# Performance work log

Hardware: AMD Instinct MI355X
Metric: run time of the kernel (lower is better)

Reference implementation:

```python
import jax, jax.numpy as jnp
import numpy as np

NUM_HEADS = 8
N_CHUNKS = 4


def _chunk_bounds(n, chunks):
    # replicate torch.chunk: chunk size = ceil(n/chunks), last chunk smaller
    cs = -(-n // chunks)
    return [min(i * cs, n) for i in range(chunks + 1)]


def setup_inputs() -> dict:
    key = jax.random.key(0)
    ks = jax.random.split(key, 9)
    dim, N, B = 512, 289, 256
    C = dim // 2
    H, d = NUM_HEADS, C // NUM_HEADS
    return {
        "x1": jax.random.normal(ks[0], (B, N, dim), jnp.float32),
        "x2": jax.random.normal(ks[1], (B, N, dim), jnp.float32),
        "W_reduce": jax.random.normal(ks[2], (dim, C), jnp.float32) * 0.02,
        "W_qkv": jax.random.normal(ks[3], (C, 3 * C), jnp.float32) * 0.02,
        "W_proj": jax.random.normal(ks[4], (C, dim), jnp.float32) * 0.02,
        "b_proj": jnp.zeros((dim,), jnp.float32),
        "w_ds": 1.0 + 0.02 * jax.random.normal(ks[5], (H, d), jnp.float32),
        "w_uds": 1.0 + 0.02 * jax.random.normal(ks[6], (H, d), jnp.float32),
        "b_uds": jnp.zeros((H, d), jnp.float32),
    }


def _branch(x, W_reduce, W_qkv, W_proj, b_proj, w_ds, w_uds, b_uds, use_ds):
    xr = x @ W_reduce                       # [B, N, C]
    B, N, C = xr.shape
    H = NUM_HEADS
    d = C // H
    scale = d ** -0.5
    qkv = (xr @ W_qkv).reshape(B, N, 3, H, d).transpose(2, 0, 3, 1, 4)  # [3,B,H,N,d]
    q, k, v = qkv[0], qkv[1], qkv[2]
    bounds = _chunk_bounds(N, N_CHUNKS)
    outs = []
    for i in range(N_CHUNKS):               # fixed 4-way chunking, per original
        s, e = bounds[i], bounds[i + 1]
        qc, kc, vc = q[:, :, s:e], k[:, :, s:e], v[:, :, s:e]
        if use_ds:
            # Distributive: learned per-head diagonal metric on head_dim, scale folded in
            attn = jnp.einsum('bhnd,bhmd->bhnm', qc * w_ds[None, :, None, :], kc) * scale
        else:
            # UnDistributive: learned per-head affine on q and k, then scaled dot-product
            qc = qc * w_uds[None, :, None, :] + b_uds[None, :, None, :]
            kc = kc * w_uds[None, :, None, :] + b_uds[None, :, None, :]
            attn = jnp.einsum('bhnd,bhmd->bhnm', qc, kc) * scale
        attn = jax.nn.softmax(attn, axis=-1)
        outs.append(jnp.einsum('bhnm,bhmd->bnhd', attn, vc))  # (attn @ v).transpose(1,2)
    o = jnp.concatenate(outs, axis=1).reshape(B, N, C)
    return o @ W_proj + b_proj


def reference(x1, x2, W_reduce, W_qkv, W_proj, b_proj, w_ds, w_uds, b_uds):
    y1 = _branch(x1, W_reduce, W_qkv, W_proj, b_proj, w_ds, w_uds, b_uds, use_ds=True)
    y2 = _branch(x2, W_reduce, W_qkv, W_proj, b_proj, w_ds, w_uds, b_uds, use_ds=False)
    return (y1, y2)
```

## Files before the change

kernel.cpp:

```cpp
#include <hip/hip_runtime.h>

typedef __bf16 bf16;
typedef bf16 bf16x4 __attribute__((ext_vector_type(4)));
typedef bf16 bf16x8 __attribute__((ext_vector_type(8)));
typedef float f32x4 __attribute__((ext_vector_type(4)));

#define LOG2E 1.4426950408889634f

__device__ __forceinline__ f32x4 mfma16(bf16x8 a, bf16x8 b, f32x4 c) {
    return __builtin_amdgcn_mfma_f32_16x16x32_bf16(a, b, c, 0, 0, 0);
}

__device__ __forceinline__ void async16(const void* g, void* l) {
    __builtin_amdgcn_global_load_lds(
        (const __attribute__((address_space(1))) void*)g,
        (__attribute__((address_space(3))) void*)l, 16, 0, 0);
}

__global__ __launch_bounds__(256) void prep_w(
    const float* __restrict__ Wr, const float* __restrict__ Wq,
    const float* __restrict__ w_ds, const float* __restrict__ w_uds,
    const float* __restrict__ b_uds,
    bf16* __restrict__ W1t, bf16* __restrict__ W2t, float* __restrict__ bias) {
    __shared__ float wq[256][17];
    const int t = threadIdx.x;
    const int k0 = blockIdx.x * 64, n0 = blockIdx.y * 16, z = blockIdx.z;
#pragma unroll
    for (int i = 0; i < 16; i++) {
        int c = i * 16 + (t >> 4);
        wq[c][t & 15] = Wq[c * 768 + n0 + (t & 15)];
    }
    __syncthreads();
    const int j = t & 15, n = n0 + j;
    const float rs = 0.17677669529663687f;
    float scale, bv;
    if (z == 0) {
        scale = (n < 256) ? w_ds[n] * rs : 1.f; bv = 0.f;
    } else if (n < 256) {
        scale = w_uds[n] * rs; bv = b_uds[n] * rs;
    } else if (n < 512) {
        scale = w_uds[n - 256]; bv = b_uds[n - 256];
    } else {
        scale = 1.f; bv = 0.f;
    }
    bf16* Wt = z ? W2t : W1t;
#pragma unroll 1
    for (int i = 0; i < 4; i++) {
        int k = k0 + (t >> 4) * 4 + i;
        float acc = 0.f;
        for (int c = 0; c < 256; c++) acc = fmaf(Wr[k * 256 + c], wq[c][j], acc);
        Wt[n * 512 + k] = (bf16)(acc * scale);
    }
    if (blockIdx.x == 0 && (t >> 4) == 0) bias[z * 768 + n] = bv;
}

__global__ void prep_wp(const float* __restrict__ Wp, bf16* __restrict__ Wpt) {
    const int n = blockIdx.x, k = threadIdx.x;
    Wpt[n * 256 + k] = (bf16)Wp[k * 512 + n];
}

__global__ __launch_bounds__(256) void gemm_qkv(
    const float* __restrict__ X, const bf16* __restrict__ Wt,
    const float* __restrict__ biasp, bf16* __restrict__ Out) {
    __shared__ __attribute__((aligned(16))) bf16 As[128 * 48];
    __shared__ __attribute__((aligned(16))) bf16 Bs[128 * 32];
    const int tid = threadIdx.x;
    const int lane = tid & 63, wave = tid >> 6;
    const int ln = lane & 15, quad = lane >> 4;
    const int bn = blockIdx.x * 128, bm = blockIdx.y * 128;
    const int wm = (wave & 1) * 64, wn = (wave >> 1) * 64;
    f32x4 acc[4][4] = {};
    float bi[4];
#pragma unroll
    for (int nt = 0; nt < 4; nt++) bi[nt] = biasp[bn + wn + nt * 16 + ln];
    const int brow = bn + wave * 32 + (lane >> 2);
    const int bcol0 = (lane & 3) * 8;
    bf16* bs_base0 = &Bs[(wave * 32) * 32];
    bf16* bs_base1 = &Bs[(wave * 32 + 16) * 32];

    for (int kb = 0; kb < 512; kb += 32) {
#pragma unroll
        for (int i = 0; i < 4; i++) {
            int idx = tid + i * 256;
            int row = idx >> 3;
            int c4 = (idx & 7) * 4;
            float4 v = *(const float4*)&X[(bm + row) * 512 + kb + c4];
            bf16x4 w = {(bf16)v.x, (bf16)v.y, (bf16)v.z, (bf16)v.w};
            *(bf16x4*)&As[row * 48 + c4] = w;
        }
        async16(&Wt[brow * 512 + kb + bcol0], bs_base0);
        async16(&Wt[(brow + 16) * 512 + kb + bcol0], bs_base1);
        __syncthreads();
        bf16x8 a[4], b[4];
#pragma unroll
        for (int mt = 0; mt < 4; mt++)
            a[mt] = *(const bf16x8*)&As[(wm + mt * 16 + ln) * 48 + quad * 8];
#pragma unroll
        for (int nt = 0; nt < 4; nt++)
            b[nt] = *(const bf16x8*)&Bs[(wn + nt * 16 + ln) * 32 + quad * 8];
#pragma unroll
        for (int mt = 0; mt < 4; mt++)
#pragma unroll
            for (int nt = 0; nt < 4; nt++)
                acc[mt][nt] = mfma16(a[mt], b[nt], acc[mt][nt]);
        __syncthreads();
    }
#pragma unroll
    for (int mt = 0; mt < 4; mt++)
#pragma unroll
        for (int nt = 0; nt < 4; nt++) {
            int col = bn + wn + nt * 16 + ln;
#pragma unroll
            for (int r = 0; r < 4; r++) {
                int row = bm + wm + mt * 16 + quad * 4 + r;
                Out[row * 768 + col] = (bf16)(acc[mt][nt][r] + bi[nt]);
            }
        }
}

__global__ __launch_bounds__(256) void gemm_proj(
    const bf16* __restrict__ A, const bf16* __restrict__ Wt,
    const float* __restrict__ bp, float* __restrict__ Y) {
    __shared__ __attribute__((aligned(16))) bf16 As[128 * 32];
    __shared__ __attribute__((aligned(16))) bf16 Bs[128 * 32];
    const int tid = threadIdx.x;
    const int lane = tid & 63, wave = tid >> 6;
    const int ln = lane & 15, quad = lane >> 4;
    const int bn = blockIdx.x * 128, bm = blockIdx.y * 128;
    const int wm = (wave & 1) * 64, wn = (wave >> 1) * 64;
    f32x4 acc[4][4] = {};
    float bi[4];
#pragma unroll
    for (int nt = 0; nt < 4; nt++) bi[nt] = bp[bn + wn + nt * 16 + ln];
    const int arow = bm + wave * 32 + (lane >> 2);
    const int brow = bn + wave * 32 + (lane >> 2);
    const int c0 = (lane & 3) * 8;
    bf16* as0 = &As[(wave * 32) * 32];
    bf16* as1 = &As[(wave * 32 + 16) * 32];
    bf16* bs0 = &Bs[(wave * 32) * 32];
    bf16* bs1 = &Bs[(wave * 32 + 16) * 32];

    for (int kb = 0; kb < 256; kb += 32) {
        async16(&A[arow * 256 + kb + c0], as0);
        async16(&A[(arow + 16) * 256 + kb + c0], as1);
        async16(&Wt[brow * 256 + kb + c0], bs0);
        async16(&Wt[(brow + 16) * 256 + kb + c0], bs1);
        __syncthreads();
        bf16x8 a[4], b[4];
#pragma unroll
        for (int mt = 0; mt < 4; mt++)
            a[mt] = *(const bf16x8*)&As[(wm + mt * 16 + ln) * 32 + quad * 8];
#pragma unroll
        for (int nt = 0; nt < 4; nt++)
            b[nt] = *(const bf16x8*)&Bs[(wn + nt * 16 + ln) * 32 + quad * 8];
#pragma unroll
        for (int mt = 0; mt < 4; mt++)
#pragma unroll
            for (int nt = 0; nt < 4; nt++)
                acc[mt][nt] = mfma16(a[mt], b[nt], acc[mt][nt]);
        __syncthreads();
    }
#pragma unroll
    for (int mt = 0; mt < 4; mt++)
#pragma unroll
        for (int nt = 0; nt < 4; nt++) {
            int col = bn + wn + nt * 16 + ln;
#pragma unroll
            for (int r = 0; r < 4; r++) {
                int row = bm + wm + mt * 16 + quad * 4 + r;
                Y[row * 512 + col] = acc[mt][nt][r] + bi[nt];
            }
        }
}

__global__ __launch_bounds__(256) void attn(const bf16* __restrict__ QKV,
                                            bf16* __restrict__ O) {
    __shared__ __attribute__((aligned(16))) bf16 vT[4][32 * 104];
    __shared__ __attribute__((aligned(16))) bf16 P[4][16 * 104];
    const int tid = threadIdx.x;
    const int lane = tid & 63, wave = tid >> 6;
    const int ln = lane & 15, quad = lane >> 4;
    const int chunk = blockIdx.x, b = blockIdx.y;
    const int s = chunk * 73;
    const int mc = min(289 - s, 73);
    const int rowbase = b * 289 + s;
    bf16* vTw = &vT[wave][0];
    bf16* Pw = &P[wave][0];
    const f32x4 zero4 = {0.f, 0.f, 0.f, 0.f};

    {
        bf16x4 z = {(bf16)0.f, (bf16)0.f, (bf16)0.f, (bf16)0.f};
        *(bf16x4*)&Pw[(lane >> 2) * 104 + 80 + (lane & 3) * 4] = z;
    }

#pragma unroll 1
    for (int hi = 0; hi < 2; hi++) {
        const int h = wave + hi * 4;
        const int cq = h * 32, ck = 256 + h * 32, cv = 512 + h * 32;

#pragma unroll
        for (int p5 = 0; p5 < 6; p5++) {
            int m = p5 * 16 + (lane >> 2);
            int mr = min(m, mc - 1);
            bf16x8 v8 = *(const bf16x8*)&QKV[(rowbase + mr) * 768 + cv + (lane & 3) * 8];
            int d0 = (lane & 3) * 8;
#pragma unroll
            for (int j = 0; j < 8; j++) vTw[(d0 + j) * 104 + m] = v8[j];
        }
        bf16x8 kf[5];
#pragma unroll
        for (int mt = 0; mt < 5; mt++) {
            int mr = min(mt * 16 + ln, mc - 1);
            kf[mt] = *(const bf16x8*)&QKV[(rowbase + mr) * 768 + ck + quad * 8];
        }
        bf16x8 vf[2][3];
#pragma unroll
        for (int dt = 0; dt < 2; dt++)
#pragma unroll
            for (int mk = 0; mk < 3; mk++)
                vf[dt][mk] = *(const bf16x8*)&vTw[(dt * 16 + ln) * 104 + mk * 32 + quad * 8];

#pragma unroll 1
        for (int nt = 0; nt < 5; nt++) {
            int qr = min(nt * 16 + ln, mc - 1);
            bf16x8 qf = *(const bf16x8*)&QKV[(rowbase + qr) * 768 + cq + quad * 8];
            f32x4 S[5];
#pragma unroll
            for (int mt = 0; mt < 5; mt++) S[mt] = mfma16(qf, kf[mt], zero4);
#pragma unroll
            for (int mt = 0; mt < 5; mt++)
                if (mt * 16 + ln >= mc) {
                    S[mt][0] = -1e30f; S[mt][1] = -1e30f;
                    S[mt][2] = -1e30f; S[mt][3] = -1e30f;
                }
            float mxv[4], sm[4];
#pragma unroll
            for (int r = 0; r < 4; r++) {
                float m0 = S[0][r];
#pragma unroll
                for (int mt = 1; mt < 5; mt++) m0 = fmaxf(m0, S[mt][r]);
                m0 = fmaxf(m0, __shfl_xor(m0, 1));
                m0 = fmaxf(m0, __shfl_xor(m0, 2));
                m0 = fmaxf(m0, __shfl_xor(m0, 4));
                m0 = fmaxf(m0, __shfl_xor(m0, 8));
                mxv[r] = m0;
                sm[r] = 0.f;
            }
#pragma unroll
            for (int mt = 0; mt < 5; mt++)
#pragma unroll
                for (int r = 0; r < 4; r++) {
                    float p = exp2f((S[mt][r] - mxv[r]) * LOG2E);
                    sm[r] += p;
                    Pw[(quad * 4 + r) * 104 + mt * 16 + ln] = (bf16)p;
                }
#pragma unroll
            for (int r = 0; r < 4; r++) {
                float t = sm[r];
                t += __shfl_xor(t, 1);
                t += __shfl_xor(t, 2);
                t += __shfl_xor(t, 4);
                t += __shfl_xor(t, 8);
                sm[r] = 1.0f / t;
            }
            f32x4 o0 = zero4, o1 = zero4;
#pragma unroll
            for (int mk = 0; mk < 3; mk++) {
                bf16x8 pa = *(const bf16x8*)&Pw[ln * 104 + mk * 32 + quad * 8];
                o0 = mfma16(pa, vf[0][mk], o0);
                o1 = mfma16(pa, vf[1][mk], o1);
            }
#pragma unroll
            for (int r = 0; r < 4; r++) {
                int nl = nt * 16 + quad * 4 + r;
                if (nl < mc) {
                    int orow = (rowbase + nl) * 256 + h * 32;
                    O[orow + ln] = (bf16)(o0[r] * sm[r]);
                    O[orow + 16 + ln] = (bf16)(o1[r] * sm[r]);
                }
            }
        }
    }
}

extern "C" void kernel_launch(void* const* d_in, const int* in_sizes, int n_in,
                              void* d_out, int out_size, void* d_ws, size_t ws_size,
                              hipStream_t stream) {
    (void)in_sizes; (void)n_in; (void)out_size;
    const float* x1 = (const float*)d_in[0];
    const float* x2 = (const float*)d_in[1];
    const float* Wr = (const float*)d_in[2];
    const float* Wq = (const float*)d_in[3];
    const float* Wp = (const float*)d_in[4];
    const float* bp = (const float*)d_in[5];
    const float* w_ds = (const float*)d_in[6];
    const float* w_uds = (const float*)d_in[7];
    const float* b_uds = (const float*)d_in[8];

    char* ws = (char*)d_ws;
    bf16* W1t = (bf16*)(ws);
    bf16* W2t = (bf16*)(ws + 786432);
    bf16* Wpt = (bf16*)(ws + 1572864);
    float* bias = (float*)(ws + 1835008);
    bf16* ob = (bf16*)(ws + 1841152);
    float* out = (float*)d_out;
    bf16* qkv;
    if (ws_size >= (size_t)39720960 + 113639424) {
        qkv = (bf16*)(ws + 39720960);
    } else {
        qkv = (bf16*)(out + 37879808);
    }

    prep_w<<<dim3(8, 48, 2), 256, 0, stream>>>(Wr, Wq, w_ds, w_uds, b_uds, W1t, W2t, bias);
    prep_wp<<<dim3(512), 256, 0, stream>>>(Wp, Wpt);
    for (int br = 0; br < 2; br++) {
        const float* X = br ? x2 : x1;
        const bf16* Wt = br ? W2t : W1t;
        gemm_qkv<<<dim3(6, 578), 256, 0, stream>>>(X, Wt, bias + br * 768, qkv);
        attn<<<dim3(4, 256), 256, 0, stream>>>(qkv, ob);
        gemm_proj<<<dim3(4, 578), 256, 0, stream>>>(ob, Wpt, bp, out + (size_t)br * 37879808);
    }
}
```

Baseline: 896.3 us.

## Double-buffer QKV and proj GEMMs with swizzled LDS and retiled QKV blocks

Both GEMMs now double-buffer their shared-memory tiles so that loads for the next k-step are issued before the MFMAs of the current step, leaving one barrier per iteration. The QKV GEMM is retiled to 64x256 blocks, with each wave owning a 64-column strip, and the launch grid is adjusted to match. LDS reads and async writes use an XOR-style rotation of the 8-element column groups to avoid bank conflicts. Launch bounds add occupancy hints, at the cost of more LDS per block and some register pressure.

After: 938.2 us. 4.7% more time.

```diff
diff --git a/kernel.cpp b/kernel.cpp
--- a/kernel.cpp
+++ b/kernel.cpp
@@ -59,11 +59,96 @@
     Wpt[n * 256 + k] = (bf16)Wp[k * 512 + n];
 }
 
-__global__ __launch_bounds__(256) void gemm_qkv(
+__global__ __launch_bounds__(256, 3) void gemm_qkv(
     const float* __restrict__ X, const bf16* __restrict__ Wt,
     const float* __restrict__ biasp, bf16* __restrict__ Out) {
-    __shared__ __attribute__((aligned(16))) bf16 As[128 * 48];
-    __shared__ __attribute__((aligned(16))) bf16 Bs[128 * 32];
+    __shared__ __attribute__((aligned(16))) bf16 As[2][64 * 40];
+    __shared__ __attribute__((aligned(16))) bf16 Bs[2][256 * 32];
+    const int tid = threadIdx.x;
+    const int lane = tid & 63, wave = tid >> 6;
+    const int ln = lane & 15, quad = lane >> 4;
+    const int bn = blockIdx.x * 256, bm = blockIdx.y * 64;
+    const int wn = wave * 64;
+    f32x4 acc[4][4] = {};
+    float bi[4];
+#pragma unroll
+    for (int nt = 0; nt < 4; nt++) bi[nt] = biasp[bn + wn + nt * 16 + ln];
+
+    const int sr = tid >> 3;
+    const int sc = (tid & 7) * 4;
+    const float* xp0 = &X[(bm + sr) * 512 + sc];
+    const float* xp1 = &X[(bm + sr + 32) * 512 + sc];
+    const int bq8 = (((lane & 3) - (lane >> 3)) & 3) * 8;
+    const int brow = bn + wn + (lane >> 2);
+    const int rq = ((quad + (ln >> 1)) & 3) * 8;
+
+    {
+        float4 v0 = *(const float4*)xp0;
+        float4 v1 = *(const float4*)xp1;
+        bf16x4 w0 = {(bf16)v0.x, (bf16)v0.y, (bf16)v0.z, (bf16)v0.w};
+        bf16x4 w1 = {(bf16)v1.x, (bf16)v1.y, (bf16)v1.z, (bf16)v1.w};
+        *(bf16x4*)&As[0][sr * 40 + sc] = w0;
+        *(bf16x4*)&As[0][(sr + 32) * 40 + sc] = w1;
+#pragma unroll
+        for (int jg = 0; jg < 4; jg++)
+            async16(&Wt[(brow + jg * 16) * 512 + bq8],
+                    &Bs[0][(wn + jg * 16) * 32]);
+    }
+    __syncthreads();
+
+    int cur = 0;
+#pragma unroll 1
+    for (int kb = 0; kb < 512; kb += 32) {
+        const int kn = kb + 32;
+        const int nxt = cur ^ 1;
+        float4 v0, v1;
+        if (kn < 512) {
+            v0 = *(const float4*)(xp0 + kn);
+            v1 = *(const float4*)(xp1 + kn);
+#pragma unroll
+            for (int jg = 0; jg < 4; jg++)
+                async16(&Wt[(brow + jg * 16) * 512 + kn + bq8],
+                        &Bs[nxt][(wn + jg * 16) * 32]);
+        }
+        bf16x8 a[4], b[4];
+#pragma unroll
+        for (int mt = 0; mt < 4; mt++)
+            a[mt] = *(const bf16x8*)&As[cur][(mt * 16 + ln) * 40 + quad * 8];
+#pragma unroll
+        for (int nt = 0; nt < 4; nt++)
+            b[nt] = *(const bf16x8*)&Bs[cur][(wn + nt * 16 + ln) * 32 + rq];
+#pragma unroll
+        for (int mt = 0; mt < 4; mt++)
+#pragma unroll
+            for (int nt = 0; nt < 4; nt++)
+                acc[mt][nt] = mfma16(a[mt], b[nt], acc[mt][nt]);
+        if (kn < 512) {
+            bf16x4 w0 = {(bf16)v0.x, (bf16)v0.y, (bf16)v0.z, (bf16)v0.w};
+            bf16x4 w1 = {(bf16)v1.x, (bf16)v1.y, (bf16)v1.z, (bf16)v1.w};
+            *(bf16x4*)&As[nxt][sr * 40 + sc] = w0;
+            *(bf16x4*)&As[nxt][(sr + 32) * 40 + sc] = w1;
+        }
+        __syncthreads();
+        cur = nxt;
+    }
+#pragma unroll
+    for (int mt = 0; mt < 4; mt++)
+#pragma unroll
+        for (int nt = 0; nt < 4; nt++) {
+            int col = bn + wn + nt * 16 + ln;
+#pragma unroll
+            for (int r = 0; r < 4; r++) {
+                int row = bm + mt * 16 + quad * 4 + r;
+                Out[row * 768 + col] = (bf16)(acc[mt][nt][r] + bi[nt]);
+            }
+        }
+}
+
+__global__ __launch_bounds__(256, 4) void gemm_proj(
+    const bf16* __restrict__ A, const bf16* __restrict__ Wt,
+    const float* __restrict__ bp, float* __restrict__ Y) {
+    __shared__ __attribute__((aligned(16))) bf16 As[2][128 * 32];
+    __shared__ __attribute__((aligned(16))) bf16 Bs[2][128 * 32];
     const int tid = threadIdx.x;
     const int lane = tid & 63, wave = tid >> 6;
     const int ln = lane & 15, quad = lane >> 4;
@@ -72,93 +157,48 @@
     f32x4 acc[4][4] = {};
     float bi[4];
 #pragma unroll
-    for (int nt = 0; nt < 4; nt++) bi[nt] = biasp[bn + wn + nt * 16 + ln];
+    for (int nt = 0; nt < 4; nt++) bi[nt] = bp[bn + wn + nt * 16 + ln];
+    const int bq8 = (((lane & 3) - (lane >> 3)) & 3) * 8;
+    const int arow = bm + wave * 32 + (lane >> 2);
     const int brow = bn + wave * 32 + (lane >> 2);
-    const int bcol0 = (lane & 3) * 8;
-    bf16* bs_base0 = &Bs[(wave * 32) * 32];
-    bf16* bs_base1 = &Bs[(wave * 32 + 16) * 32];
-
-    for (int kb = 0; kb < 512; kb += 32) {
-#pragma unroll
-        for (int i = 0; i < 4; i++) {
-            int idx = tid + i * 256;
-            int row = idx >> 3;
-            int c4 = (idx & 7) * 4;
-            float4 v = *(const float4*)&X[(bm + row) * 512 + kb + c4];
-            bf16x4 w = {(bf16)v.x, (bf16)v.y, (bf16)v.z, (bf16)v.w};
-            *(bf16x4*)&As[row * 48 + c4] = w;
-        }
-        async16(&Wt[brow * 512 + kb + bcol0], bs_base0);
-        async16(&Wt[(brow + 16) * 512 + kb + bcol0], bs_base1);
-        __syncthreads();
+    const int rq = ((quad + (ln >> 1)) & 3) * 8;
+    bf16* as0 = &As[0][(wave * 32) * 32];
+    bf16* as1 = &As[0][(wave * 32 + 16) * 32];
+    bf16* bs0 = &Bs[0][(wave * 32) * 32];
+    bf16* bs1 = &Bs[0][(wave * 32 + 16) * 32];
+    const int bufstride = 128 * 32;
+
+    async16(&A[arow * 256 + bq8], as0);
+    async16(&A[(arow + 16) * 256 + bq8], as1);
+    async16(&Wt[brow * 256 + bq8], bs0);
+    async16(&Wt[(brow + 16) * 256 + bq8], bs1);
+    __syncthreads();
+
+    int cur = 0;
+#pragma unroll 1
+    for (int kb = 0; kb < 256; kb += 32) {
+        const int kn = kb + 32;
+        const int nxt = cur ^ 1;
+        if (kn < 256) {
+            async16(&A[arow * 256 + kn + bq8], as0 + nxt * bufstride);
+            async16(&A[(arow + 16) * 256 + kn + bq8], as1 + nxt * bufstride);
+            async16(&Wt[brow * 256 + kn + bq8], bs0 + nxt * bufstride);
+            async16(&Wt[(brow + 16) * 256 + kn + bq8], bs1 + nxt * bufstride);
+        }
         bf16x8 a[4], b[4];
 #pragma unroll
         for (int mt = 0; mt < 4; mt++)
-            a[mt] = *(const bf16x8*)&As[(wm + mt * 16 + ln) * 48 + quad * 8];
+            a[mt] = *(const bf16x8*)&As[cur][(wm + mt * 16 + ln) * 32 + rq];
 #pragma unroll
         for (int nt = 0; nt < 4; nt++)
-            b[nt] = *(const bf16x8*)&Bs[(wn + nt * 16 + ln) * 32 + quad * 8];
+            b[nt] = *(const bf16x8*)&Bs[cur][(wn + nt * 16 + ln) * 32 + rq];
 #pragma unroll
         for (int mt = 0; mt < 4; mt++)
 #pragma unroll
             for (int nt = 0; nt < 4; nt++)
                 acc[mt][nt] = mfma16(a[mt], b[nt], acc[mt][nt]);
         __syncthreads();
-    }
-#pragma unroll
-    for (int mt = 0; mt < 4; mt++)
-#pragma unroll
-        for (int nt = 0; nt < 4; nt++) {
-            int col = bn + wn + nt * 16 + ln;
-#pragma unroll
-            for (int r = 0; r < 4; r++) {
-                int row = bm + wm + mt * 16 + quad * 4 + r;
-                Out[row * 768 + col] = (bf16)(acc[mt][nt][r] + bi[nt]);
-            }
-        }
-}
-
-__global__ __launch_bounds__(256) void gemm_proj(
-    const bf16* __restrict__ A, const bf16* __restrict__ Wt,
-    const float* __restrict__ bp, float* __restrict__ Y) {
-    __shared__ __attribute__((aligned(16))) bf16 As[128 * 32];
-    __shared__ __attribute__((aligned(16))) bf16 Bs[128 * 32];
-    const int tid = threadIdx.x;
-    const int lane = tid & 63, wave = tid >> 6;
-    const int ln = lane & 15, quad = lane >> 4;
-    const int bn = blockIdx.x * 128, bm = blockIdx.y * 128;
-    const int wm = (wave & 1) * 64, wn = (wave >> 1) * 64;
-    f32x4 acc[4][4] = {};
-    float bi[4];
-#pragma unroll
-    for (int nt = 0; nt < 4; nt++) bi[nt] = bp[bn + wn + nt * 16 + ln];
-    const int arow = bm + wave * 32 + (lane >> 2);
-    const int brow = bn + wave * 32 + (lane >> 2);
-    const int c0 = (lane & 3) * 8;
-    bf16* as0 = &As[(wave * 32) * 32];
-    bf16* as1 = &As[(wave * 32 + 16) * 32];
-    bf16* bs0 = &Bs[(wave * 32) * 32];
-    bf16* bs1 = &Bs[(wave * 32 + 16) * 32];
-
-    for (int kb = 0; kb < 256; kb += 32) {
-        async16(&A[arow * 256 + kb + c0], as0);
-        async16(&A[(arow + 16) * 256 + kb + c0], as1);
-        async16(&Wt[brow * 256 + kb + c0], bs0);
-        async16(&Wt[(brow + 16) * 256 + kb + c0], bs1);
-        __syncthreads();
-        bf16x8 a[4], b[4];
-#pragma unroll
-        for (int mt = 0; mt < 4; mt++)
-            a[mt] = *(const bf16x8*)&As[(wm + mt * 16 + ln) * 32 + quad * 8];
-#pragma unroll
-        for (int nt = 0; nt < 4; nt++)
-            b[nt] = *(const bf16x8*)&Bs[(wn + nt * 16 + ln) * 32 + quad * 8];
-#pragma unroll
-        for (int mt = 0; mt < 4; mt++)
-#pragma unroll
-            for (int nt = 0; nt < 4; nt++)
-                acc[mt][nt] = mfma16(a[mt], b[nt], acc[mt][nt]);
-        __syncthreads();
+        cur = nxt;
     }
 #pragma unroll
     for (int mt = 0; mt < 4; mt++)
@@ -316,7 +356,7 @@
     for (int br = 0; br < 2; br++) {
         const float* X = br ? x2 : x1;
         const bf16* Wt = br ? W2t : W1t;
-        gemm_qkv<<<dim3(6, 578), 256, 0, stream>>>(X, Wt, bias + br * 768, qkv);
+        gemm_qkv<<<dim3(3, 1156), 256, 0, stream>>>(X, Wt, bias + br * 768, qkv);
         attn<<<dim3(4, 256), 256, 0, stream>>>(qkv, ob);
         gemm_proj<<<dim3(4, 578), 256, 0, stream>>>(ob, Wpt, bp, out + (size_t)br * 37879808);
     }
```

## Pre-cast inputs to bf16 and double-buffer GEMM tiles with async LDS loads

Applied to the files above, without the earlier changes.

Adds an xcast kernel that converts both fp32 inputs to bf16 once, staging them in the output buffer. The QKV GEMM can then load A tiles with async global-to-LDS copies instead of converting in registers. Both GEMMs now use double-buffered LDS: the next k-slice is prefetched while the current one feeds the MFMAs, leaving one barrier per iteration, and both get an occupancy hint in launch_bounds. The launches are reordered so the second branch's QKV GEMM runs before the first branch's projection. The cost is an extra full pass over both inputs and more LDS per block.

Result: no change. 902.0 us (+0.6%).

```diff
diff --git a/kernel.cpp b/kernel.cpp
--- a/kernel.cpp
+++ b/kernel.cpp
@@ -59,11 +59,28 @@
     Wpt[n * 256 + k] = (bf16)Wp[k * 512 + n];
 }
 
-__global__ __launch_bounds__(256) void gemm_qkv(
-    const float* __restrict__ X, const bf16* __restrict__ Wt,
+__global__ __launch_bounds__(256) void xcast(const float* __restrict__ X1,
+                                             const float* __restrict__ X2,
+                                             bf16* __restrict__ O1,
+                                             bf16* __restrict__ O2) {
+    const float* X = blockIdx.y ? X2 : X1;
+    bf16* O = blockIdx.y ? O2 : O1;
+    const long total = 37879808;
+    const long stride = (long)gridDim.x * 256 * 8;
+    for (long i = ((long)blockIdx.x * 256 + threadIdx.x) * 8; i < total; i += stride) {
+        float4 a = *(const float4*)&X[i];
+        float4 b = *(const float4*)&X[i + 4];
+        bf16x8 w = {(bf16)a.x, (bf16)a.y, (bf16)a.z, (bf16)a.w,
+                    (bf16)b.x, (bf16)b.y, (bf16)b.z, (bf16)b.w};
+        *(bf16x8*)&O[i] = w;
+    }
+}
+
+__global__ __launch_bounds__(256, 4) void gemm_qkv(
+    const bf16* __restrict__ X, const bf16* __restrict__ Wt,
     const float* __restrict__ biasp, bf16* __restrict__ Out) {
-    __shared__ __attribute__((aligned(16))) bf16 As[128 * 48];
-    __shared__ __attribute__((aligned(16))) bf16 Bs[128 * 32];
+    __shared__ __attribute__((aligned(16))) bf16 As[2][128 * 32];
+    __shared__ __attribute__((aligned(16))) bf16 Bs[2][128 * 32];
     const int tid = threadIdx.x;
     const int lane = tid & 63, wave = tid >> 6;
     const int ln = lane & 15, quad = lane >> 4;
@@ -73,37 +90,46 @@
     float bi[4];
 #pragma unroll
     for (int nt = 0; nt < 4; nt++) bi[nt] = biasp[bn + wn + nt * 16 + ln];
+    const int arow = bm + wave * 32 + (lane >> 2);
     const int brow = bn + wave * 32 + (lane >> 2);
-    const int bcol0 = (lane & 3) * 8;
-    bf16* bs_base0 = &Bs[(wave * 32) * 32];
-    bf16* bs_base1 = &Bs[(wave * 32 + 16) * 32];
-
+    const int c0 = (lane & 3) * 8;
+    bf16* as0 = &As[0][(wave * 32) * 32];
+    bf16* as1 = &As[0][(wave * 32 + 16) * 32];
+    bf16* bs0 = &Bs[0][(wave * 32) * 32];
+    bf16* bs1 = &Bs[0][(wave * 32 + 16) * 32];
+    const int bufstride = 128 * 32;
+
+    async16(&X[arow * 512 + c0], as0);
+    async16(&X[(arow + 16) * 512 + c0], as1);
+    async16(&Wt[brow * 512 + c0], bs0);
+    async16(&Wt[(brow + 16) * 512 + c0], bs1);
+    __syncthreads();
+
+    int cur = 0;
+#pragma unroll 1
     for (int kb = 0; kb < 512; kb += 32) {
-#pragma unroll
-        for (int i = 0; i < 4; i++) {
-            int idx = tid + i * 256;
-            int row = idx >> 3;
-            int c4 = (idx & 7) * 4;
-            float4 v = *(const float4*)&X[(bm + row) * 512 + kb + c4];
-            bf16x4 w = {(bf16)v.x, (bf16)v.y, (bf16)v.z, (bf16)v.w};
-            *(bf16x4*)&As[row * 48 + c4] = w;
-        }
-        async16(&Wt[brow * 512 + kb + bcol0], bs_base0);
-        async16(&Wt[(brow + 16) * 512 + kb + bcol0], bs_base1);
-        __syncthreads();
+        const int kn = kb + 32;
+        const int nxt = cur ^ 1;
+        if (kn < 512) {
+            async16(&X[arow * 512 + kn + c0], as0 + nxt * bufstride);
+            async16(&X[(arow + 16) * 512 + kn + c0], as1 + nxt * bufstride);
+            async16(&Wt[brow * 512 + kn + c0], bs0 + nxt * bufstride);
+            async16(&Wt[(brow + 16) * 512 + kn + c0], bs1 + nxt * bufstride);
+        }
         bf16x8 a[4], b[4];
 #pragma unroll
         for (int mt = 0; mt < 4; mt++)
-            a[mt] = *(const bf16x8*)&As[(wm + mt * 16 + ln) * 48 + quad * 8];
+            a[mt] = *(const bf16x8*)&As[cur][(wm + mt * 16 + ln) * 32 + quad * 8];
 #pragma unroll
         for (int nt = 0; nt < 4; nt++)
-            b[nt] = *(const bf16x8*)&Bs[(wn + nt * 16 + ln) * 32 + quad * 8];
+            b[nt] = *(const bf16x8*)&Bs[cur][(wn + nt * 16 + ln) * 32 + quad * 8];
 #pragma unroll
         for (int mt = 0; mt < 4; mt++)
 #pragma unroll
             for (int nt = 0; nt < 4; nt++)
                 acc[mt][nt] = mfma16(a[mt], b[nt], acc[mt][nt]);
         __syncthreads();
+        cur = nxt;
     }
 #pragma unroll
     for (int mt = 0; mt < 4; mt++)
@@ -118,11 +144,11 @@
         }
 }
 
-__global__ __launch_bounds__(256) void gemm_proj(
+__global__ __launch_bounds__(256, 4) void gemm_proj(
     const bf16* __restrict__ A, const bf16* __restrict__ Wt,
     const float* __restrict__ bp, float* __restrict__ Y) {
-    __shared__ __attribute__((aligned(16))) bf16 As[128 * 32];
-    __shared__ __attribute__((aligned(16))) bf16 Bs[128 * 32];
+    __shared__ __attribute__((aligned(16))) bf16 As[2][128 * 32];
+    __shared__ __attribute__((aligned(16))) bf16 Bs[2][128 * 32];
     const int tid = threadIdx.x;
     const int lane = tid & 63, wave = tid >> 6;
     const int ln = lane & 15, quad = lane >> 4;
@@ -135,30 +161,43 @@
     const int arow = bm + wave * 32 + (lane >> 2);
     const int brow = bn + wave * 32 + (lane >> 2);
     const int c0 = (lane & 3) * 8;
-    bf16* as0 = &As[(wave * 32) * 32];
-    bf16* as1 = &As[(wave * 32 + 16) * 32];
-    bf16* bs0 = &Bs[(wave * 32) * 32];
-    bf16* bs1 = &Bs[(wave * 32 + 16) * 32];
-
+    bf16* as0 = &As[0][(wave * 32) * 32];
+    bf16* as1 = &As[0][(wave * 32 + 16) * 32];
+    bf16* bs0 = &Bs[0][(wave * 32) * 32];
+    bf16* bs1 = &Bs[0][(wave * 32 + 16) * 32];
+    const int bufstride = 128 * 32;
+
+    async16(&A[arow * 256 + c0], as0);
+    async16(&A[(arow + 16) * 256 + c0], as1);
+    async16(&Wt[brow * 256 + c0], bs0);
+    async16(&Wt[(brow + 16) * 256 + c0], bs1);
+    __syncthreads();
+
+    int cur = 0;
+#pragma unroll 1
     for (int kb = 0; kb < 256; kb += 32) {
-        async16(&A[arow * 256 + kb + c0], as0);
-        async16(&A[(arow + 16) * 256 + kb + c0], as1);
-        async16(&Wt[brow * 256 + kb + c0], bs0);
-        async16(&Wt[(brow + 16) * 256 + kb + c0], bs1);
-        __syncthreads();
+        const int kn = kb + 32;
+        const int nxt = cur ^ 1;
+        if (kn < 256) {
+            async16(&A[arow * 256 + kn + c0], as0 + nxt * bufstride);
+            async16(&A[(arow + 16) * 256 + kn + c0], as1 + nxt * bufstride);
+            async16(&Wt[brow * 256 + kn + c0], bs0 + nxt * bufstride);
+            async16(&Wt[(brow + 16) * 256 + kn + c0], bs1 + nxt * bufstride);
+        }
         bf16x8 a[4], b[4];
 #pragma unroll
         for (int mt = 0; mt < 4; mt++)
-            a[mt] = *(const bf16x8*)&As[(wm + mt * 16 + ln) * 32 + quad * 8];
+            a[mt] = *(const bf16x8*)&As[cur][(wm + mt * 16 + ln) * 32 + quad * 8];
 #pragma unroll
         for (int nt = 0; nt < 4; nt++)
-            b[nt] = *(const bf16x8*)&Bs[(wn + nt * 16 + ln) * 32 + quad * 8];
+            b[nt] = *(const bf16x8*)&Bs[cur][(wn + nt * 16 + ln) * 32 + quad * 8];
 #pragma unroll
         for (int mt = 0; mt < 4; mt++)
 #pragma unroll
             for (int nt = 0; nt < 4; nt++)
                 acc[mt][nt] = mfma16(a[mt], b[nt], acc[mt][nt]);
         __syncthreads();
+        cur = nxt;
     }
 #pragma unroll
     for (int mt = 0; mt < 4; mt++)
@@ -286,7 +325,7 @@
 extern "C" void kernel_launch(void* const* d_in, const int* in_sizes, int n_in,
                               void* d_out, int out_size, void* d_ws, size_t ws_size,
                               hipStream_t stream) {
-    (void)in_sizes; (void)n_in; (void)out_size;
+    (void)in_sizes; (void)n_in; (void)out_size; (void)ws_size;
     const float* x1 = (const float*)d_in[0];
     const float* x2 = (const float*)d_in[1];
     const float* Wr = (const float*)d_in[2];
@@ -304,20 +343,19 @@
     float* bias = (float*)(ws + 1835008);
     bf16* ob = (bf16*)(ws + 1841152);
     float* out = (float*)d_out;
-    bf16* qkv;
-    if (ws_size >= (size_t)39720960 + 113639424) {
-        qkv = (bf16*)(ws + 39720960);
-    } else {
-        qkv = (bf16*)(out + 37879808);
-    }
+    char* outc = (char*)d_out;
+    bf16* Xb1 = (bf16*)(outc);
+    bf16* Xb2 = (bf16*)(outc + 75759616);
+    bf16* qkv = (bf16*)(outc + 151519232);
 
     prep_w<<<dim3(8, 48, 2), 256, 0, stream>>>(Wr, Wq, w_ds, w_uds, b_uds, W1t, W2t, bias);
     prep_wp<<<dim3(512), 256, 0, stream>>>(Wp, Wpt);
-    for (int br = 0; br < 2; br++) {
-        const float* X = br ? x2 : x1;
-        const bf16* Wt = br ? W2t : W1t;
-        gemm_qkv<<<dim3(6, 578), 256, 0, stream>>>(X, Wt, bias + br * 768, qkv);
-        attn<<<dim3(4, 256), 256, 0, stream>>>(qkv, ob);
-        gemm_proj<<<dim3(4, 578), 256, 0, stream>>>(ob, Wpt, bp, out + (size_t)br * 37879808);
-    }
-}
+    xcast<<<dim3(2048, 2), 256, 0, stream>>>(x1, x2, Xb1, Xb2);
+
+    gemm_qkv<<<dim3(6, 578), 256, 0, stream>>>(Xb1, W1t, bias, qkv);
+    attn<<<dim3(4, 256), 256, 0, stream>>>(qkv, ob);
+    gemm_qkv<<<dim3(6, 578), 256, 0, stream>>>(Xb2, W2t, bias + 768, qkv);
+    gemm_proj<<<dim3(4, 578), 256, 0, stream>>>(ob, Wpt, bp, out);
+    attn<<<dim3(4, 256), 256, 0, stream>>>(qkv, ob);
+    gemm_proj<<<dim3(4, 578), 256, 0, stream>>>(ob, Wpt, bp, out + (size_t)37879808);
+}
```
